# Optimization experiments

Hardware: AMD Instinct MI355X
Metric: run time of the kernel (lower is better)

The kernel has to match this reference:

```python
import jax, jax.numpy as jnp
import numpy as np

B, S, H = 16, 4096, 1024   # batch, subword len, encoder hidden (roberta-large)
N, DW = 2048, 50           # max word tokens, glove word-emb size (hardcoded 50 in module)
NEG = -jnp.inf


def setup_inputs() -> dict:
    key = jax.random.key(0)
    k1, k2 = jax.random.split(key)
    context_emb = jax.random.normal(k1, (B, S, H), dtype=jnp.float32)
    word_emb = jax.random.normal(k2, (B, N, DW), dtype=jnp.float32)
    # build a realistic subword->word mapping: each example has ns_b words,
    # words 0..ns_b-2 own contiguous subword spans covering all S subwords
    # (word ns_b-1 is the special doc token handled via map[ns-1]=range(ns-1)).
    rng = np.random.default_rng(0)
    ns_np = rng.integers(N // 2, N + 1, size=(B,)).astype(np.int32)
    pos = np.arange(S)
    seg_np = np.empty((B, S), dtype=np.int32)
    for b in range(B):
        nw = int(ns_np[b]) - 1  # words with real subword spans
        seg_np[b] = np.minimum((pos * nw) // S, nw - 1)
    return {
        "context_emb": context_emb,
        "word_emb": word_emb,
        "seg_ids": jnp.asarray(seg_np),
        "ns": jnp.asarray(ns_np),
    }


def _forward(context_emb, word_emb, seg_ids, ns):
    # ragged span max-pool: subword -> word via segment_max (fused, no python loops)
    seg_max = jax.vmap(
        lambda c, s: jax.ops.segment_max(c, s, num_segments=N + 1, indices_are_sorted=True)
    )(context_emb, seg_ids)[:, :N]                              # [B, N, H]

    spos = jnp.arange(S)
    wpos = jnp.arange(N)
    # last word token (tok_id = ns-1): map[ns-1] = range(ns-1) -> max over subwords 0..ns-2
    last_ctx_mask = spos[None, :] < (ns[:, None] - 1)            # [B, S]
    last_ctx = jnp.max(jnp.where(last_ctx_mask[..., None], context_emb, NEG), axis=1)  # [B, H]
    # word-emb part of last token: max over word_emb[i, 0:ns]
    wmask = wpos[None, :] < ns[:, None]                          # [B, N]
    last_w = jnp.max(jnp.where(wmask[..., None], word_emb, NEG), axis=1)               # [B, DW]

    is_last = wpos[None, :] == (ns[:, None] - 1)                 # [B, N]
    ctx_part = jnp.where(is_last[..., None], last_ctx[:, None, :], seg_max)
    w_part = jnp.where(is_last[..., None], last_w[:, None, :], word_emb)
    out = jnp.concatenate([ctx_part, w_part], axis=-1)           # [B, N, H+DW]
    # padding word positions (tok_id >= ns) are zero vectors in the original
    return jnp.where(wmask[..., None], out, 0.0)


def reference(context_emb, word_emb, seg_ids, ns):
    return _forward(context_emb, word_emb, seg_ids, ns)
```

## Files before the change

### kernel.cpp

```cpp
#include <hip/hip_runtime.h>

#define BB 16
#define SS 4096
#define HH 1024
#define NW 2048
#define DWW 50
#define OUTW (HH + DWW)
#define CHUNKS 32
#define CHUNK 64
#define SEGSLICE (SS / CHUNKS)

#define WS_START_OFF   0
#define WS_PARTIAL_OFF (BB * NW * 4)
#define WS_LASTWP_OFF  (WS_PARTIAL_OFF + BB * CHUNKS * HH * 4)

__global__ __launch_bounds__(256) void k_pre(
    const float* __restrict__ ctx, const float* __restrict__ wemb,
    const int* __restrict__ seg, const int* __restrict__ ns,
    int* __restrict__ start, float* __restrict__ partial,
    float* __restrict__ lastwp) {
  const int c = blockIdx.x;
  const int b = blockIdx.y;
  const int t = threadIdx.x;
  const int nsb = ns[b];

  const int* segb = seg + b * SS;
  int* sb = start + b * NW;
  const int sbase = c * SEGSLICE;
  if (t < SEGSLICE) {
    const int s = sbase + t;
    const int v = segb[s];
    if (s == 0 || segb[s - 1] != v) sb[v] = s;
  }

  {
    const int d = t & 63;
    const int r = t >> 6;
    float m = -INFINITY;
    if (d < DWW) {
      const float* wb = wemb + (size_t)b * NW * DWW;
      for (int i = 0; i < CHUNK / 4; ++i) {
        const int w = c * CHUNK + 4 * i + r;
        if (w < nsb) m = fmaxf(m, wb[(size_t)w * DWW + d]);
      }
    }
    __shared__ float red[256];
    red[t] = m;
    __syncthreads();
    if (r == 0 && d < DWW) {
      lastwp[((size_t)b * CHUNKS + c) * 64 + d] =
          fmaxf(fmaxf(red[d], red[64 + d]), fmaxf(red[128 + d], red[192 + d]));
    }
  }

  {
    const int lim = nsb - 1;
    const int s0 = c * CHUNK;
    const int s1 = min(s0 + CHUNK, lim);
    float4 m = make_float4(-INFINITY, -INFINITY, -INFINITY, -INFINITY);
    const float* cb = ctx + (size_t)b * SS * HH;
    for (int s = s0; s < s1; ++s) {
      const float4 v = *reinterpret_cast<const float4*>(cb + (size_t)s * HH + 4 * t);
      m.x = fmaxf(m.x, v.x);
      m.y = fmaxf(m.y, v.y);
      m.z = fmaxf(m.z, v.z);
      m.w = fmaxf(m.w, v.w);
    }
    float4* p = reinterpret_cast<float4*>(partial + ((size_t)b * CHUNKS + c) * HH);
    p[t] = m;
  }
}

__global__ __launch_bounds__(256) void k_main(
    const float* __restrict__ ctx, const float* __restrict__ wemb,
    const int* __restrict__ ns, const int* __restrict__ start,
    const float* __restrict__ partial, const float* __restrict__ lastwp,
    float* __restrict__ out) {
  const int w = blockIdx.x;
  const int b = blockIdx.y;
  const int t = threadIdx.x;
  const int nsb = ns[b];
  float* orow = out + ((size_t)b * NW + w) * OUTW;

  if (w >= nsb) {
    float2* o2 = reinterpret_cast<float2*>(orow);
    for (int j = t; j < OUTW / 2; j += 256) o2[j] = make_float2(0.0f, 0.0f);
    return;
  }

  float4 m = make_float4(-INFINITY, -INFINITY, -INFINITY, -INFINITY);
  if (w == nsb - 1) {
    const float* p = partial + (size_t)b * CHUNKS * HH;
    for (int c = 0; c < CHUNKS; ++c) {
      const float4 v = *reinterpret_cast<const float4*>(p + (size_t)c * HH + 4 * t);
      m.x = fmaxf(m.x, v.x);
      m.y = fmaxf(m.y, v.y);
      m.z = fmaxf(m.z, v.z);
      m.w = fmaxf(m.w, v.w);
    }
  } else {
    const int s0 = start[b * NW + w];
    const int s1 = (w == nsb - 2) ? SS : start[b * NW + w + 1];
    const float* cb = ctx + (size_t)b * SS * HH;
    for (int s = s0; s < s1; ++s) {
      const float4 v = *reinterpret_cast<const float4*>(cb + (size_t)s * HH + 4 * t);
      m.x = fmaxf(m.x, v.x);
      m.y = fmaxf(m.y, v.y);
      m.z = fmaxf(m.z, v.z);
      m.w = fmaxf(m.w, v.w);
    }
  }

  float2* o2 = reinterpret_cast<float2*>(orow);
  o2[2 * t]     = make_float2(m.x, m.y);
  o2[2 * t + 1] = make_float2(m.z, m.w);

  if (t < DWW) {
    float v;
    if (w == nsb - 1) {
      float mm = -INFINITY;
      const float* lp = lastwp + (size_t)b * CHUNKS * 64;
      for (int c = 0; c < CHUNKS; ++c) mm = fmaxf(mm, lp[c * 64 + t]);
      v = mm;
    } else {
      v = wemb[((size_t)b * NW + w) * DWW + t];
    }
    orow[HH + t] = v;
  }
}

extern "C" void kernel_launch(void* const* d_in, const int* in_sizes, int n_in,
                              void* d_out, int out_size, void* d_ws, size_t ws_size,
                              hipStream_t stream) {
  const float* ctx  = (const float*)d_in[0];
  const float* wemb = (const float*)d_in[1];
  const int*   seg  = (const int*)d_in[2];
  const int*   ns   = (const int*)d_in[3];
  float* out = (float*)d_out;

  char* ws = (char*)d_ws;
  int*   start   = (int*)(ws + WS_START_OFF);
  float* partial = (float*)(ws + WS_PARTIAL_OFF);
  float* lastwp  = (float*)(ws + WS_LASTWP_OFF);

  k_pre<<<dim3(CHUNKS, BB), dim3(256), 0, stream>>>(ctx, wemb, seg, ns, start, partial, lastwp);
  k_main<<<dim3(NW, BB), dim3(256), 0, stream>>>(ctx, wemb, ns, start, partial, lastwp, out);
}
```

Before: 436.6 us.

## Merge partial reductions into main kernel and find spans by binary search

The separate pre-pass that built a span-start table and computed the last-token partial maxima is removed. Each word block now finds its subword span by binary-searching the sorted segment ids, and the last-token partial reductions run as extra blocks inside the main grid, so they overlap with the per-word work. A small tail kernel combines the partials for the last-token row. The aim is to remove the serial dependency between the pre-pass and the main pass. The cost is roughly 24 dependent segment-id loads per block for the two binary searches.

Result: no change. 442.7 us (+1.4%).

```diff
diff --git a/kernel.cpp b/kernel.cpp
--- a/kernel.cpp
+++ b/kernel.cpp
@@ -8,78 +8,68 @@
 #define OUTW (HH + DWW)
 #define CHUNKS 32
 #define CHUNK 64
-#define SEGSLICE (SS / CHUNKS)
 
-#define WS_START_OFF   0
-#define WS_PARTIAL_OFF (BB * NW * 4)
-#define WS_LASTWP_OFF  (WS_PARTIAL_OFF + BB * CHUNKS * HH * 4)
+#define WS_PARTIAL_OFF 0
+#define WS_LASTWP_OFF  (BB * CHUNKS * HH * 4)
 
-__global__ __launch_bounds__(256) void k_pre(
-    const float* __restrict__ ctx, const float* __restrict__ wemb,
-    const int* __restrict__ seg, const int* __restrict__ ns,
-    int* __restrict__ start, float* __restrict__ partial,
-    float* __restrict__ lastwp) {
-  const int c = blockIdx.x;
-  const int b = blockIdx.y;
-  const int t = threadIdx.x;
-  const int nsb = ns[b];
-
-  const int* segb = seg + b * SS;
-  int* sb = start + b * NW;
-  const int sbase = c * SEGSLICE;
-  if (t < SEGSLICE) {
-    const int s = sbase + t;
-    const int v = segb[s];
-    if (s == 0 || segb[s - 1] != v) sb[v] = s;
+__device__ __forceinline__ int lower_bound_seg(const int* __restrict__ segb, int x) {
+  int lo = 0, hi = SS;
+  while (lo < hi) {
+    int mid = (lo + hi) >> 1;
+    if (segb[mid] < x) lo = mid + 1; else hi = mid;
   }
-
-  {
-    const int d = t & 63;
-    const int r = t >> 6;
-    float m = -INFINITY;
-    if (d < DWW) {
-      const float* wb = wemb + (size_t)b * NW * DWW;
-      for (int i = 0; i < CHUNK / 4; ++i) {
-        const int w = c * CHUNK + 4 * i + r;
-        if (w < nsb) m = fmaxf(m, wb[(size_t)w * DWW + d]);
-      }
-    }
-    __shared__ float red[256];
-    red[t] = m;
-    __syncthreads();
-    if (r == 0 && d < DWW) {
-      lastwp[((size_t)b * CHUNKS + c) * 64 + d] =
-          fmaxf(fmaxf(red[d], red[64 + d]), fmaxf(red[128 + d], red[192 + d]));
-    }
-  }
-
-  {
-    const int lim = nsb - 1;
-    const int s0 = c * CHUNK;
-    const int s1 = min(s0 + CHUNK, lim);
-    float4 m = make_float4(-INFINITY, -INFINITY, -INFINITY, -INFINITY);
-    const float* cb = ctx + (size_t)b * SS * HH;
-    for (int s = s0; s < s1; ++s) {
-      const float4 v = *reinterpret_cast<const float4*>(cb + (size_t)s * HH + 4 * t);
-      m.x = fmaxf(m.x, v.x);
-      m.y = fmaxf(m.y, v.y);
-      m.z = fmaxf(m.z, v.z);
-      m.w = fmaxf(m.w, v.w);
-    }
-    float4* p = reinterpret_cast<float4*>(partial + ((size_t)b * CHUNKS + c) * HH);
-    p[t] = m;
-  }
+  return lo;
 }
 
 __global__ __launch_bounds__(256) void k_main(
     const float* __restrict__ ctx, const float* __restrict__ wemb,
-    const int* __restrict__ ns, const int* __restrict__ start,
-    const float* __restrict__ partial, const float* __restrict__ lastwp,
+    const int* __restrict__ seg, const int* __restrict__ ns,
+    float* __restrict__ partial, float* __restrict__ lastwp,
     float* __restrict__ out) {
-  const int w = blockIdx.x;
   const int b = blockIdx.y;
   const int t = threadIdx.x;
   const int nsb = ns[b];
+  const float* cb = ctx + (size_t)b * SS * HH;
+
+  if (blockIdx.x >= NW) {
+    const int c = blockIdx.x - NW;
+
+    {
+      const int d = t & 63;
+      const int r = t >> 6;
+      float m = -INFINITY;
+      if (d < DWW) {
+        const float* wb = wemb + (size_t)b * NW * DWW;
+        for (int i = 0; i < CHUNK / 4; ++i) {
+          const int w = c * CHUNK + 4 * i + r;
+          if (w < nsb) m = fmaxf(m, wb[(size_t)w * DWW + d]);
+        }
+      }
+      __shared__ float red[256];
+      red[t] = m;
+      __syncthreads();
+      if (r == 0 && d < DWW) {
+        lastwp[((size_t)b * CHUNKS + c) * 64 + d] =
+            fmaxf(fmaxf(red[d], red[64 + d]), fmaxf(red[128 + d], red[192 + d]));
+      }
+    }
+
+    {
+      const int s0 = c * CHUNK;
+      const int s1 = min(s0 + CHUNK, nsb - 1);
+      float4 m = make_float4(-INFINITY, -INFINITY, -INFINITY, -INFINITY);
+      for (int s = s0; s < s1; ++s) {
+        const float4 v = *reinterpret_cast<const float4*>(cb + (size_t)s * HH + 4 * t);
+        m.x = fmaxf(m.x, v.x); m.y = fmaxf(m.y, v.y);
+        m.z = fmaxf(m.z, v.z); m.w = fmaxf(m.w, v.w);
+      }
+      float4* p = reinterpret_cast<float4*>(partial + ((size_t)b * CHUNKS + c) * HH);
+      p[t] = m;
+    }
+    return;
+  }
+
+  const int w = blockIdx.x;
   float* orow = out + ((size_t)b * NW + w) * OUTW;
 
   if (w >= nsb) {
@@ -87,44 +77,43 @@
     for (int j = t; j < OUTW / 2; j += 256) o2[j] = make_float2(0.0f, 0.0f);
     return;
   }
+  if (w == nsb - 1) return;
+
+  const int* segb = seg + b * SS;
+  const int s0 = lower_bound_seg(segb, w);
+  const int s1 = lower_bound_seg(segb, w + 1);
 
   float4 m = make_float4(-INFINITY, -INFINITY, -INFINITY, -INFINITY);
-  if (w == nsb - 1) {
-    const float* p = partial + (size_t)b * CHUNKS * HH;
-    for (int c = 0; c < CHUNKS; ++c) {
-      const float4 v = *reinterpret_cast<const float4*>(p + (size_t)c * HH + 4 * t);
-      m.x = fmaxf(m.x, v.x);
-      m.y = fmaxf(m.y, v.y);
-      m.z = fmaxf(m.z, v.z);
-      m.w = fmaxf(m.w, v.w);
-    }
-  } else {
-    const int s0 = start[b * NW + w];
-    const int s1 = (w == nsb - 2) ? SS : start[b * NW + w + 1];
-    const float* cb = ctx + (size_t)b * SS * HH;
-    for (int s = s0; s < s1; ++s) {
-      const float4 v = *reinterpret_cast<const float4*>(cb + (size_t)s * HH + 4 * t);
-      m.x = fmaxf(m.x, v.x);
-      m.y = fmaxf(m.y, v.y);
-      m.z = fmaxf(m.z, v.z);
-      m.w = fmaxf(m.w, v.w);
-    }
+  for (int s = s0; s < s1; ++s) {
+    const float4 v = *reinterpret_cast<const float4*>(cb + (size_t)s * HH + 4 * t);
+    m.x = fmaxf(m.x, v.x); m.y = fmaxf(m.y, v.y);
+    m.z = fmaxf(m.z, v.z); m.w = fmaxf(m.w, v.w);
   }
 
   float2* o2 = reinterpret_cast<float2*>(orow);
   o2[2 * t]     = make_float2(m.x, m.y);
   o2[2 * t + 1] = make_float2(m.z, m.w);
 
+  if (t < DWW) orow[HH + t] = wemb[((size_t)b * NW + w) * DWW + t];
+}
+
+__global__ __launch_bounds__(1024) void k_last(
+    const int* __restrict__ ns, const float* __restrict__ partial,
+    const float* __restrict__ lastwp, float* __restrict__ out) {
+  const int b = blockIdx.x;
+  const int t = threadIdx.x;
+  const int nsb = ns[b];
+  float* orow = out + ((size_t)b * NW + (nsb - 1)) * OUTW;
+
+  float m = -INFINITY;
+  const float* p = partial + (size_t)b * CHUNKS * HH;
+  for (int c = 0; c < CHUNKS; ++c) m = fmaxf(m, p[c * HH + t]);
+  orow[t] = m;
+
   if (t < DWW) {
-    float v;
-    if (w == nsb - 1) {
-      float mm = -INFINITY;
-      const float* lp = lastwp + (size_t)b * CHUNKS * 64;
-      for (int c = 0; c < CHUNKS; ++c) mm = fmaxf(mm, lp[c * 64 + t]);
-      v = mm;
-    } else {
-      v = wemb[((size_t)b * NW + w) * DWW + t];
-    }
+    float v = -INFINITY;
+    const float* lp = lastwp + (size_t)b * CHUNKS * 64;
+    for (int c = 0; c < CHUNKS; ++c) v = fmaxf(v, lp[c * 64 + t]);
     orow[HH + t] = v;
   }
 }
@@ -139,10 +128,9 @@
   float* out = (float*)d_out;
 
   char* ws = (char*)d_ws;
-  int*   start   = (int*)(ws + WS_START_OFF);
   float* partial = (float*)(ws + WS_PARTIAL_OFF);
   float* lastwp  = (float*)(ws + WS_LASTWP_OFF);
 
-  k_pre<<<dim3(CHUNKS, BB), dim3(256), 0, stream>>>(ctx, wemb, seg, ns, start, partial, lastwp);
-  k_main<<<dim3(NW, BB), dim3(256), 0, stream>>>(ctx, wemb, ns, start, partial, lastwp, out);
+  k_main<<<dim3(NW + CHUNKS, BB), dim3(256), 0, stream>>>(ctx, wemb, seg, ns, partial, lastwp, out);
+  k_last<<<dim3(BB), dim3(1024), 0, stream>>>(ns, partial, lastwp, out);
 }
```
